# Performance work log

Measured on AMD Instinct MI355X. Metric: run time of the kernel, lower is better.

## Reference

```python
import jax, jax.numpy as jnp
import numpy as np


def _conv(x, w, stride=1, pad=0):
    return jax.lax.conv_general_dilated(
        x, w, window_strides=(stride, stride),
        padding=[(pad, pad), (pad, pad)],
        dimension_numbers=('NCHW', 'OIHW', 'NCHW'))


def _frozen_bn(x, gamma, beta, mean, var):
    # FrozenBatchNorm2d: scale = gamma * rsqrt(var); bias = beta - mean*scale
    scale = gamma * jax.lax.rsqrt(var)
    bias = beta - mean * scale
    return x * scale[None, :, None, None] + bias[None, :, None, None]


def setup_inputs() -> dict:
    key = jax.random.key(0)
    ks = jax.random.split(key, 16)
    N, Cin, H, W = 32, 1024, 28, 28
    Cb, Cout = 256, 1024
    x = jax.random.normal(ks[0], (N, Cin, H, W), dtype=jnp.float32)
    # conv weights, kaiming-uniform-ish scale
    w1 = jax.random.uniform(ks[1], (Cb, Cin, 1, 1), minval=-1, maxval=1) * (1.0 / np.sqrt(Cin))
    w2 = jax.random.uniform(ks[2], (Cb, Cb, 3, 3), minval=-1, maxval=1) * (1.0 / np.sqrt(Cb * 9))
    w3 = jax.random.uniform(ks[3], (Cout, Cb, 1, 1), minval=-1, maxval=1) * (1.0 / np.sqrt(Cb))
    def bn_params(k, n):
        k1, k2, k3, k4 = jax.random.split(k, 4)
        gamma = jax.random.uniform(k1, (n,), minval=0.5, maxval=1.5)
        beta = jax.random.normal(k2, (n,)) * 0.1
        mean = jax.random.normal(k3, (n,)) * 0.1
        var = jax.random.uniform(k4, (n,), minval=0.5, maxval=1.5)
        return gamma, beta, mean, var
    g1, b1, m1, v1 = bn_params(ks[4], Cb)
    g2, b2, m2, v2 = bn_params(ks[5], Cb)
    g3, b3, m3, v3 = bn_params(ks[6], Cout)
    return dict(x=x, w1=w1, w2=w2, w3=w3,
                g1=g1, b1=b1, m1=m1, v1=v1,
                g2=g2, b2=b2, m2=m2, v2=v2,
                g3=g3, b3=b3, m3=m3, v3=v3)


def reference(x, w1, w2, w3, g1, b1, m1, v1, g2, b2, m2, v2, g3, b3, m3, v3):
    identity = x
    out = _conv(x, w1, stride=1, pad=0)          # 1x1: Cin -> Cb
    out = jax.nn.relu(_frozen_bn(out, g1, b1, m1, v1))
    out = _conv(out, w2, stride=1, pad=1)        # 3x3: Cb -> Cb
    out = jax.nn.relu(_frozen_bn(out, g2, b2, m2, v2))
    out = _conv(out, w3, stride=1, pad=0)        # 1x1: Cb -> Cout
    out = _frozen_bn(out, g3, b3, m3, v3)
    # stride==1 and in_channels==out_channels -> downsample is None
    out = jax.nn.relu(out + identity)
    return out
```

## Files before the change

### kernel.cpp

```cpp
#include <hip/hip_runtime.h>


#define BK 64
#define WAITVM(N) asm volatile("s_waitcnt vmcnt(" #N ")" ::: "memory")

typedef __attribute__((ext_vector_type(8))) short short8;
typedef __attribute__((ext_vector_type(4))) float f32x4;

__device__ inline unsigned short f2bf(float f) {
    unsigned int u = __float_as_uint(f);
    u += 0x7fff + ((u >> 16) & 1);
    return (unsigned short)(u >> 16);
}

__device__ inline void gload16(const unsigned short* g, unsigned short* l) {
    __builtin_amdgcn_global_load_lds(
        (const __attribute__((address_space(1))) unsigned int*)g,
        (__attribute__((address_space(3))) unsigned int*)l, 16, 0, 0);
}

__global__ __launch_bounds__(256) void prep_w(
    const float* __restrict__ w1, const float* __restrict__ w2, const float* __restrict__ w3,
    const float* g1, const float* b1, const float* m1, const float* v1,
    const float* g2, const float* b2, const float* m2, const float* v2,
    const float* g3, const float* b3, const float* m3, const float* v3,
    unsigned short* __restrict__ Wb1, unsigned short* __restrict__ Wt2,
    unsigned short* __restrict__ Wb3,
    float* __restrict__ bn1, float* __restrict__ bn2, float* __restrict__ bn3) {
    int i = blockIdx.x * 256 + threadIdx.x;
    if (i < 262144) Wb1[i] = f2bf(w1[i]);
    if (i < 589824) {
        int kw = i % 3, t1 = i / 3;
        int kh = t1 % 3, t2 = t1 / 3;
        int ci = t2 & 255, co = t2 >> 8;
        Wt2[(size_t)((kh * 3 + kw) * 256 + co) * 256 + ci] = f2bf(w2[i]);
    }
    if (i < 262144) Wb3[i] = f2bf(w3[i]);
    if (i < 256) { float s = g1[i] * rsqrtf(v1[i]); bn1[i] = s; bn1[256 + i] = b1[i] - m1[i] * s; }
    if (i < 256) { float s = g2[i] * rsqrtf(v2[i]); bn2[i] = s; bn2[256 + i] = b2[i] - m2[i] * s; }
    if (i < 1024) { float s = g3[i] * rsqrtf(v3[i]); bn3[i] = s; bn3[1024 + i] = b3[i] - m3[i] * s; }
}

__global__ __launch_bounds__(256) void border_zero(uint4* __restrict__ y1p) {
    int i = blockIdx.x * 256 + threadIdx.x;
    int ch8 = i & 31;
    int t = i >> 5;
    int cell = t % 116;
    int n = t / 116;
    int h, w;
    if (cell < 30)      { h = 0;          w = cell; }
    else if (cell < 60) { h = 29;         w = cell - 30; }
    else if (cell < 88) { h = cell - 59;  w = 0; }
    else                { h = cell - 87;  w = 29; }
    y1p[((size_t)n * 900 + h * 30 + w) * 32 + ch8] = make_uint4(0u, 0u, 0u, 0u);
}

template <int CX, int NTAPS, int LAYER, int NT, int BMT>
__device__ __forceinline__ void conv_body(
    const float* __restrict__ Xf,
    const unsigned short* __restrict__ Xg, const unsigned short* __restrict__ Wg,
    const float* __restrict__ bn, int nco,
    const float* __restrict__ residual,
    unsigned short* __restrict__ obf, float* __restrict__ ofp) {
    constexpr int KSTEPS = CX / BK;
    constexpr int NSTEP = NTAPS * KSTEPS;
    constexpr int XB = BMT * BK * 2;
    constexpr int WB = NT * BK * 2;
    constexpr int STAGEB = 2 * (XB + WB);
    constexpr int EPIB = (LAYER == 3) ? 64 * 132 * 4 : 64 * (NT + 8) * 2;
    constexpr int SMEMB = STAGEB > EPIB ? STAGEB : EPIB;
    constexpr int NWJ = BMT / 32;
    constexpr int WR = NT / 32;
    constexpr int XR = BMT / 32;

    __shared__ __align__(16) char smem[SMEMB];
    unsigned short* const Xs0 = (unsigned short*)smem;
    unsigned short* const Xs1 = (unsigned short*)(smem + XB);
    unsigned short* const Ws0 = (unsigned short*)(smem + 2 * XB);
    unsigned short* const Ws1 = (unsigned short*)(smem + 2 * XB + WB);

    const int tid = threadIdx.x;
    const int wave = tid >> 6, lane = tid & 63;
    const int quad = lane >> 4, l15 = lane & 15;
    const int Pb = blockIdx.x * BMT;
    const int cb = blockIdx.y * NT;
    const int wco = (wave & 1) * 64;
    const int wpx = (wave >> 1) * (BMT / 2);

    size_t wro[WR];
    #pragma unroll
    for (int t = 0; t < WR; ++t) {
        int slot = t * 256 + tid;
        int row = slot >> 3;
        int c = slot & 7;
        wro[t] = (size_t)(cb + row) * CX + ((c ^ (row & 7)) * 8);
    }

    int cso[4];
    size_t xrow[4];
    if (LAYER != 1) {
        #pragma unroll
        for (int t = 0; t < XR; ++t) {
            int slot = t * 256 + tid;
            int row = slot >> 3;
            int c = slot & 7;
            cso[t] = ((c ^ (row & 7)) * 8);
            if (LAYER == 2) {
                int P = Pb + row;
                int n = P / 784, rem = P - n * 784;
                int h = rem / 28, w = rem - h * 28;
                xrow[t] = (size_t)n * 900 + h * 30 + w;
            } else {
                xrow[t] = (size_t)(Pb + row);
            }
        }
    }

    const int cpl = (lane >> 2) + (wave & 1) * 16;
    size_t xbase[2];
    int plr[2];
    if (LAYER == 1) {
        #pragma unroll
        for (int r = 0; r < 2; ++r) {
            int quarter = (wave >> 1) + 2 * r;
            int pl = quarter * 16 + (lane & 3) * 4;
            int P = Pb + pl;
            int n = P / 784, p = P - n * 784;
            plr[r] = pl;
            xbase[r] = ((size_t)n * 1024 + 2 * cpl) * 784 + p;
        }
    }

    auto stageW = [&](int s, unsigned short* wsb) {
        int tap = (NTAPS == 1) ? 0 : (s / KSTEPS);
        int k0 = (s - tap * KSTEPS) * BK;
        const unsigned short* Wtap = Wg + (size_t)tap * 256 * CX;
        #pragma unroll
        for (int t = 0; t < WR; ++t)
            gload16(Wtap + wro[t] + k0, wsb + (t * 256 + wave * 64) * 8);
    };
    auto stageX = [&](int s, unsigned short* xsb) {
        int tap = (NTAPS == 1) ? 0 : (s / KSTEPS);
        int k0 = (s - tap * KSTEPS) * BK;
        int tapofs = (NTAPS == 9) ? ((tap / 3) * 30 + (tap % 3)) : 0;
        #pragma unroll
        for (int t = 0; t < XR; ++t)
            gload16(Xg + (xrow[t] + tapofs) * (size_t)CX + k0 + cso[t],
                    xsb + (t * 256 + wave * 64) * 8);
    };
    float4 xa[2], xb[2];
    auto loadX1 = [&](int s) {
        size_t k0 = (size_t)s * BK;
        #pragma unroll
        for (int r = 0; r < 2; ++r) {
            const float* src = Xf + xbase[r] + k0 * 784;
            xa[r] = *(const float4*)src;
            xb[r] = *(const float4*)(src + 784);
        }
    };
    auto convW1 = [&](unsigned short* xsb) {
        #pragma unroll
        for (int r = 0; r < 2; ++r) {
            float av[4] = {xa[r].x, xa[r].y, xa[r].z, xa[r].w};
            float bv[4] = {xb[r].x, xb[r].y, xb[r].z, xb[r].w};
            #pragma unroll
            for (int j = 0; j < 4; ++j) {
                unsigned u = (unsigned)f2bf(av[j]) | ((unsigned)f2bf(bv[j]) << 16);
                int row = plr[r] + j;
                int dw = row * 32 + (((cpl >> 2) ^ (row & 7)) << 2) + (cpl & 3);
                ((unsigned*)xsb)[dw] = u;
            }
        }
    };

    f32x4 acc[4][NWJ];
    #pragma unroll
    for (int i = 0; i < 4; ++i)
        #pragma unroll
        for (int j = 0; j < NWJ; ++j)
            acc[i][j] = (f32x4){0.f, 0.f, 0.f, 0.f};

    auto compute = [&](const unsigned short* xsb, const unsigned short* wsb) {
        #pragma unroll
        for (int kk = 0; kk < BK; kk += 32) {
            short8 af[4], bf[NWJ];
            const int cbase = kk >> 3;
            #pragma unroll
            for (int wi = 0; wi < 4; ++wi) {
                int row = wco + wi * 16 + l15;
                int ch = (cbase + quad) ^ (row & 7);
                af[wi] = *(const short8*)(wsb + (row * 8 + ch) * 8);
            }
            #pragma unroll
            for (int wj = 0; wj < NWJ; ++wj) {
                int row = wpx + wj * 16 + l15;
                int ch = (cbase + quad) ^ (row & 7);
                bf[wj] = *(const short8*)(xsb + (row * 8 + ch) * 8);
            }
            #pragma unroll
            for (int wi = 0; wi < 4; ++wi)
                #pragma unroll
                for (int wj = 0; wj < NWJ; ++wj)
                    acc[wi][wj] = __builtin_amdgcn_mfma_f32_16x16x32_bf16(
                        af[wi], bf[wj], acc[wi][wj], 0, 0, 0);
        }
    };

    if (LAYER == 1) loadX1(0);
    stageW(0, Ws0);
    if (LAYER == 1) convW1(Xs0);
    else            stageX(0, Xs0);

    int cur = 0;
    #pragma unroll 1
    for (int s = 0; s < NSTEP; ++s) {
        unsigned short* xc = cur ? Xs1 : Xs0;
        unsigned short* wc = cur ? Ws1 : Ws0;
        unsigned short* xn = cur ? Xs0 : Xs1;
        unsigned short* wn = cur ? Ws0 : Ws1;
        const bool pre = (s + 1 < NSTEP);
        if (pre) {
            if (LAYER == 1) loadX1(s + 1);
            stageW(s + 1, wn);
            if (LAYER != 1) stageX(s + 1, xn);
        }
        if (pre) {
            if constexpr (LAYER == 2) WAITVM(6);
            else                      WAITVM(8);
        } else {
            WAITVM(0);
        }
        __builtin_amdgcn_sched_barrier(0);
        __builtin_amdgcn_s_barrier();
        compute(xc, wc);
        if (LAYER == 1 && pre) convW1(xn);
        if (LAYER == 1) asm volatile("s_waitcnt lgkmcnt(0)" ::: "memory");
        __builtin_amdgcn_s_barrier();
        __builtin_amdgcn_sched_barrier(0);
        cur ^= 1;
    }

    __syncthreads();

    if (LAYER == 3) {
        float* ep = (float*)smem;
        #pragma unroll
        for (int pass = 0; pass < 2; ++pass) {
            if ((wave & 1) == pass) {
                #pragma unroll
                for (int wi = 0; wi < 4; ++wi) {
                    int co0 = cb + wco + wi * 16 + quad * 4;
                    f32x4 sc = *(const f32x4*)(bn + co0);
                    f32x4 bi = *(const f32x4*)(bn + nco + co0);
                    int cr0 = wi * 16 + quad * 4;
                    #pragma unroll
                    for (int wj = 0; wj < 4; ++wj) {
                        int px = wpx + wj * 16 + l15;
                        #pragma unroll
                        for (int r = 0; r < 4; ++r)
                            ep[(cr0 + r) * 132 + px] = fmaf(acc[wi][wj][r], sc[r], bi[r]);
                    }
                }
            }
            __syncthreads();
            {
                int cr = tid >> 2;
                int cg = tid & 3;
                int co = cb + pass * 64 + cr;
                #pragma unroll
                for (int k = 0; k < 8; ++k) {
                    int px4 = (cg + 4 * k) * 4;
                    f32x4 v = *(const f32x4*)(ep + cr * 132 + px4);
                    int P = Pb + px4;
                    int n = P / 784, p = P - n * 784;
                    size_t off = ((size_t)n * 1024 + co) * 784 + p;
                    float4 rs = *(const float4*)(residual + off);
                    float4 o;
                    o.x = v[0] + rs.x; o.x = o.x > 0.f ? o.x : 0.f;
                    o.y = v[1] + rs.y; o.y = o.y > 0.f ? o.y : 0.f;
                    o.z = v[2] + rs.z; o.z = o.z > 0.f ? o.z : 0.f;
                    o.w = v[3] + rs.w; o.w = o.w > 0.f ? o.w : 0.f;
                    *(float4*)(ofp + off) = o;
                }
            }
            __syncthreads();
        }
    } else {
        constexpr int EPW = NT + 8;
        unsigned short* ep = (unsigned short*)smem;
        #pragma unroll
        for (int wi = 0; wi < 4; ++wi) {
            int co0 = cb + wco + wi * 16 + quad * 4;
            f32x4 sc = *(const f32x4*)(bn + co0);
            f32x4 bi = *(const f32x4*)(bn + nco + co0);
            int col = wco + wi * 16 + quad * 4;
            #pragma unroll
            for (int wj = 0; wj < NWJ; ++wj) {
                int pxl = wpx + wj * 16 + l15;
                float v0 = fmaf(acc[wi][wj][0], sc[0], bi[0]); v0 = v0 > 0.f ? v0 : 0.f;
                float v1 = fmaf(acc[wi][wj][1], sc[1], bi[1]); v1 = v1 > 0.f ? v1 : 0.f;
                float v2 = fmaf(acc[wi][wj][2], sc[2], bi[2]); v2 = v2 > 0.f ? v2 : 0.f;
                float v3 = fmaf(acc[wi][wj][3], sc[3], bi[3]); v3 = v3 > 0.f ? v3 : 0.f;
                uint2 pk;
                pk.x = (unsigned)f2bf(v0) | ((unsigned)f2bf(v1) << 16);
                pk.y = (unsigned)f2bf(v2) | ((unsigned)f2bf(v3) << 16);
                *(uint2*)(ep + pxl * EPW + col) = pk;
            }
        }
        __syncthreads();
        {
            int pxl = tid >> 2;
            int cg = tid & 3;
            int P = Pb + pxl;
            size_t orow;
            if (LAYER == 1) {
                int n = P / 784, rem = P - n * 784;
                int h = rem / 28, w = rem - h * 28;
                orow = (size_t)n * 900 + (h + 1) * 30 + (w + 1);
            } else {
                orow = (size_t)P;
            }
            #pragma unroll
            for (int k = 0; k < NT / 32; ++k) {
                int cc = (cg + 4 * k) * 8;
                uint4 v = *(const uint4*)(ep + pxl * EPW + cc);
                *(uint4*)(obf + orow * 256 + cb + cc) = v;
            }
        }
    }
}

__global__ __launch_bounds__(256) void conv1_mfma(
    const float* __restrict__ Xf, const unsigned short* __restrict__ Wg,
    const float* __restrict__ bn, unsigned short* __restrict__ obf) {
    conv_body<1024, 1, 1, 128, 64>(Xf, nullptr, Wg, bn, 256, nullptr, obf, nullptr);
}
__global__ __launch_bounds__(256) void conv2_mfma(
    const unsigned short* __restrict__ Xg, const unsigned short* __restrict__ Wg,
    const float* __restrict__ bn, unsigned short* __restrict__ obf) {
    conv_body<256, 9, 2, 128, 64>(nullptr, Xg, Wg, bn, 256, nullptr, obf, nullptr);
}
__global__ __launch_bounds__(256) void conv3_mfma(
    const unsigned short* __restrict__ Xg, const unsigned short* __restrict__ Wg,
    const float* __restrict__ bn, const float* __restrict__ residual,
    float* __restrict__ ofp) {
    conv_body<256, 1, 3, 128, 128>(nullptr, Xg, Wg, bn, 1024, residual, nullptr, ofp);
}

extern "C" void kernel_launch(void* const* d_in, const int* in_sizes, int n_in,
                              void* d_out, int out_size, void* d_ws, size_t ws_size,
                              hipStream_t stream) {
    const float* x  = (const float*)d_in[0];
    const float* w1 = (const float*)d_in[1];
    const float* w2 = (const float*)d_in[2];
    const float* w3 = (const float*)d_in[3];
    const float* g1 = (const float*)d_in[4];  const float* b1 = (const float*)d_in[5];
    const float* m1 = (const float*)d_in[6];  const float* v1 = (const float*)d_in[7];
    const float* g2 = (const float*)d_in[8];  const float* b2 = (const float*)d_in[9];
    const float* m2 = (const float*)d_in[10]; const float* v2 = (const float*)d_in[11];
    const float* g3 = (const float*)d_in[12]; const float* b3 = (const float*)d_in[13];
    const float* m3 = (const float*)d_in[14]; const float* v3 = (const float*)d_in[15];
    float* out = (float*)d_out;

    char* ws = (char*)d_ws;
    unsigned short* y1p = (unsigned short*)(ws);
    unsigned short* y2  = (unsigned short*)(ws + 14745600);
    unsigned short* Wb1 = (unsigned short*)(ws + 27590656);
    unsigned short* Wt2 = (unsigned short*)(ws + 28114944);
    unsigned short* Wb3 = (unsigned short*)(ws + 29294592);
    float* bn1 = (float*)(ws + 29818880);
    float* bn2 = (float*)(ws + 29820928);
    float* bn3 = (float*)(ws + 29822976);

    prep_w<<<2304, 256, 0, stream>>>(w1, w2, w3,
                                     g1, b1, m1, v1, g2, b2, m2, v2, g3, b3, m3, v3,
                                     Wb1, Wt2, Wb3, bn1, bn2, bn3);
    border_zero<<<464, 256, 0, stream>>>((uint4*)y1p);

    conv1_mfma<<<dim3(392, 2), 256, 0, stream>>>(x, Wb1, bn1, y1p);
    conv2_mfma<<<dim3(392, 2), 256, 0, stream>>>(y1p, Wt2, bn2, y2);
    conv3_mfma<<<dim3(196, 8), 256, 0, stream>>>(y2, Wb3, bn3, x, out);
}
```

Measured before the change: 319.0 us.

## Fold border zeroing into prep kernel, remap conv block order, use packed bf16 converts

```diff
diff --git a/kernel.cpp b/kernel.cpp
--- a/kernel.cpp
+++ b/kernel.cpp
@@ -1,4 +1,5 @@
 #include <hip/hip_runtime.h>
+#include <hip/hip_bf16.h>
 
 
 #define BK 64
@@ -11,6 +12,11 @@
     unsigned int u = __float_as_uint(f);
     u += 0x7fff + ((u >> 16) & 1);
     return (unsigned short)(u >> 16);
+}
+
+__device__ inline unsigned cvt_pk_bf16(float a, float b) {
+    __hip_bfloat162 h = __float22bfloat162_rn(make_float2(a, b));
+    return *reinterpret_cast<unsigned*>(&h);
 }
 
 __device__ inline void gload16(const unsigned short* g, unsigned short* l) {
@@ -26,7 +32,8 @@
     const float* g3, const float* b3, const float* m3, const float* v3,
     unsigned short* __restrict__ Wb1, unsigned short* __restrict__ Wt2,
     unsigned short* __restrict__ Wb3,
-    float* __restrict__ bn1, float* __restrict__ bn2, float* __restrict__ bn3) {
+    float* __restrict__ bn1, float* __restrict__ bn2, float* __restrict__ bn3,
+    uint4* __restrict__ y1p) {
     int i = blockIdx.x * 256 + threadIdx.x;
     if (i < 262144) Wb1[i] = f2bf(w1[i]);
     if (i < 589824) {
@@ -39,20 +46,18 @@
     if (i < 256) { float s = g1[i] * rsqrtf(v1[i]); bn1[i] = s; bn1[256 + i] = b1[i] - m1[i] * s; }
     if (i < 256) { float s = g2[i] * rsqrtf(v2[i]); bn2[i] = s; bn2[256 + i] = b2[i] - m2[i] * s; }
     if (i < 1024) { float s = g3[i] * rsqrtf(v3[i]); bn3[i] = s; bn3[1024 + i] = b3[i] - m3[i] * s; }
-}
-
-__global__ __launch_bounds__(256) void border_zero(uint4* __restrict__ y1p) {
-    int i = blockIdx.x * 256 + threadIdx.x;
-    int ch8 = i & 31;
-    int t = i >> 5;
-    int cell = t % 116;
-    int n = t / 116;
-    int h, w;
-    if (cell < 30)      { h = 0;          w = cell; }
-    else if (cell < 60) { h = 29;         w = cell - 30; }
-    else if (cell < 88) { h = cell - 59;  w = 0; }
-    else                { h = cell - 87;  w = 29; }
-    y1p[((size_t)n * 900 + h * 30 + w) * 32 + ch8] = make_uint4(0u, 0u, 0u, 0u);
+    if (i < 118784) {
+        int ch8 = i & 31;
+        int t = i >> 5;
+        int cell = t % 116;
+        int n = t / 116;
+        int h, w;
+        if (cell < 30)      { h = 0;          w = cell; }
+        else if (cell < 60) { h = 29;         w = cell - 30; }
+        else if (cell < 88) { h = cell - 59;  w = 0; }
+        else                { h = cell - 87;  w = 29; }
+        y1p[((size_t)n * 900 + h * 30 + w) * 32 + ch8] = make_uint4(0u, 0u, 0u, 0u);
+    }
 }
 
 template <int CX, int NTAPS, int LAYER, int NT, int BMT>
@@ -82,8 +87,12 @@
     const int tid = threadIdx.x;
     const int wave = tid >> 6, lane = tid & 63;
     const int quad = lane >> 4, l15 = lane & 15;
-    const int Pb = blockIdx.x * BMT;
-    const int cb = blockIdx.y * NT;
+
+    int bx, by;
+    if (LAYER == 3) { bx = blockIdx.x; by = blockIdx.y; }
+    else            { int b = blockIdx.x; bx = (b >> 4) * 8 + (b & 7); by = (b >> 3) & 1; }
+    const int Pb = bx * BMT;
+    const int cb = by * NT;
     const int wco = (wave & 1) * 64;
     const int wpx = (wave >> 1) * (BMT / 2);
 
@@ -165,7 +174,7 @@
             float bv[4] = {xb[r].x, xb[r].y, xb[r].z, xb[r].w};
             #pragma unroll
             for (int j = 0; j < 4; ++j) {
-                unsigned u = (unsigned)f2bf(av[j]) | ((unsigned)f2bf(bv[j]) << 16);
+                unsigned u = cvt_pk_bf16(av[j], bv[j]);
                 int row = plr[r] + j;
                 int dw = row * 32 + (((cpl >> 2) ^ (row & 7)) << 2) + (cpl & 3);
                 ((unsigned*)xsb)[dw] = u;
@@ -302,8 +311,8 @@
                 float v2 = fmaf(acc[wi][wj][2], sc[2], bi[2]); v2 = v2 > 0.f ? v2 : 0.f;
                 float v3 = fmaf(acc[wi][wj][3], sc[3], bi[3]); v3 = v3 > 0.f ? v3 : 0.f;
                 uint2 pk;
-                pk.x = (unsigned)f2bf(v0) | ((unsigned)f2bf(v1) << 16);
-                pk.y = (unsigned)f2bf(v2) | ((unsigned)f2bf(v3) << 16);
+                pk.x = cvt_pk_bf16(v0, v1);
+                pk.y = cvt_pk_bf16(v2, v3);
                 *(uint2*)(ep + pxl * EPW + col) = pk;
             }
         }
@@ -374,10 +383,9 @@
 
     prep_w<<<2304, 256, 0, stream>>>(w1, w2, w3,
                                      g1, b1, m1, v1, g2, b2, m2, v2, g3, b3, m3, v3,
-                                     Wb1, Wt2, Wb3, bn1, bn2, bn3);
-    border_zero<<<464, 256, 0, stream>>>((uint4*)y1p);
-
-    conv1_mfma<<<dim3(392, 2), 256, 0, stream>>>(x, Wb1, bn1, y1p);
-    conv2_mfma<<<dim3(392, 2), 256, 0, stream>>>(y1p, Wt2, bn2, y2);
+                                     Wb1, Wt2, Wb3, bn1, bn2, bn3, (uint4*)y1p);
+
+    conv1_mfma<<<784, 256, 0, stream>>>(x, Wb1, bn1, y1p);
+    conv2_mfma<<<784, 256, 0, stream>>>(y1p, Wt2, bn2, y2);
     conv3_mfma<<<dim3(196, 8), 256, 0, stream>>>(y2, Wb3, bn3, x, out);
 }
```

After: 322.5 us. No clear change (+1.1%).
